# Kernel optimization log

Hardware: AMD Instinct MI355X
Metric: run time of the kernel (lower is better)

## Reference

```python
import jax, jax.numpy as jnp
import numpy as np

N = 100_000   # nodes
E = 1_600_000 # edges per graph
D = 64        # feature width
HA = 32       # attention hidden


def setup_inputs() -> dict:
    key = jax.random.key(0)
    ks = jax.random.split(key, 20)
    inp = {}
    inp["h"] = jax.random.normal(ks[0], (N, D), jnp.float32)
    inp["e_od"] = jax.random.normal(ks[1], (E, D), jnp.float32)
    inp["e_ad"] = jax.random.normal(ks[2], (E, D), jnp.float32)
    inp["src_od"] = jax.random.randint(ks[3], (E,), 0, N)
    inp["dst_od"] = jax.random.randint(ks[4], (E,), 0, N)
    inp["src_ad"] = jax.random.randint(ks[5], (E,), 0, N)
    inp["dst_ad"] = jax.random.randint(ks[6], (E,), 0, N)
    s = 1.0 / np.sqrt(D).astype(np.float32)
    # stacked params: index 0 = OD graph, index 1 = AD graph
    inp["W_src"]  = jax.random.normal(ks[7],  (2, D, D), jnp.float32) * s
    inp["W_dst"]  = jax.random.normal(ks[8],  (2, D, D), jnp.float32) * s
    inp["W_edge"] = jax.random.normal(ks[9],  (2, D, D), jnp.float32) * s
    inp["b_msg"]  = jnp.zeros((2, D), jnp.float32)
    inp["W_self"] = jax.random.normal(ks[10], (2, D, D), jnp.float32) * s
    inp["W_agg"]  = jax.random.normal(ks[11], (2, D, D), jnp.float32) * s
    inp["b_node"] = jnp.zeros((2, D), jnp.float32)
    # Attention (Aggregate_samedim): Linear(D->HA, bias) -> tanh -> Linear(HA->1, no bias)
    inp["attn_l1_w"] = jax.random.normal(ks[12], (D, HA), jnp.float32) * s
    inp["attn_l1_b"] = jnp.zeros((HA,), jnp.float32)
    inp["attn_l2_w"] = jax.random.normal(ks[13], (HA, 1), jnp.float32) * (1.0 / np.sqrt(HA).astype(np.float32))
    return inp


def reference(h, e_od, e_ad, src_od, dst_od, src_ad, dst_ad,
              W_src, W_dst, W_edge, b_msg, W_self, W_agg, b_node,
              attn_l1_w, attn_l1_b, attn_l2_w):
    def mpnn(i, e, src, dst):
        # edge message: gather src/dst node feats, small GEMMs, relu  [E, D]
        m = jax.nn.relu(h[src] @ W_src[i] + h[dst] @ W_dst[i] + e @ W_edge[i] + b_msg[i])
        # scatter-sum to destination nodes  [N, D]
        agg = jax.ops.segment_sum(m, dst, num_segments=N)
        # node update  [N, D]
        return jax.nn.relu(h @ W_self[i] + agg @ W_agg[i] + b_node[i])

    intra = mpnn(0, e_od, src_od, dst_od)  # OD graph node states
    inter = mpnn(1, e_ad, src_ad, dst_ad)  # AD graph node states
    # Aggregate_samedim: attention over the 2-way stack
    rep = jnp.stack([intra, inter], axis=1)               # [N, 2, D]
    w = jnp.tanh(rep @ attn_l1_w + attn_l1_b) @ attn_l2_w  # [N, 2, 1]
    beta = jax.nn.softmax(w, axis=1)
    return (beta * rep).sum(axis=1)                        # [N, D]
```

## Files before the change

kernel.cpp:

```cpp
#include <hip/hip_runtime.h>
#include <hip/hip_bf16.h>

using short8  = __attribute__((ext_vector_type(8))) short;
using ushort8 = __attribute__((ext_vector_type(8))) unsigned short;
using f32x4   = __attribute__((ext_vector_type(4))) float;
using fvec4   = __attribute__((ext_vector_type(4))) float;

#define CH 8192
#define XST 72

__device__ inline unsigned short f2bf(float x) {
  union { __hip_bfloat16 b; unsigned short u; } c;
  c.b = __float2bfloat16(x);
  return c.u;
}
__device__ inline float bf2f(unsigned short s) {
  return __uint_as_float(((unsigned int)s) << 16);
}
__device__ inline unsigned int pk2(float lo, float hi) {
  union { __hip_bfloat162 b; unsigned int u; } c;
  c.b = __float22bfloat162_rn(make_float2(lo, hi));
  return c.u;
}
__device__ inline short8 cvt8(fvec4 a, fvec4 b) {
  union { short8 s; unsigned int u[4]; } r;
  r.u[0] = pk2(a[0], a[1]);
  r.u[1] = pk2(a[2], a[3]);
  r.u[2] = pk2(b[0], b[1]);
  r.u[3] = pk2(b[2], b[3]);
  return r.s;
}

__device__ inline void load_bfrags_f32(const float* __restrict__ W, short8 bfr[2][4], int lane) {
  int l15 = lane & 15, lh = lane >> 4;
#pragma unroll
  for (int ks = 0; ks < 2; ++ks)
#pragma unroll
    for (int ct = 0; ct < 4; ++ct) {
      short8 v;
#pragma unroll
      for (int i = 0; i < 8; ++i)
        v[i] = (short)f2bf(W[(ks * 32 + lh * 8 + i) * 64 + ct * 16 + l15]);
      bfr[ks][ct] = v;
    }
}

__device__ inline void load_bfrags(const unsigned short* __restrict__ Wf, short8 bfr[2][4], int lane) {
#pragma unroll
  for (int ks = 0; ks < 2; ++ks)
#pragma unroll
    for (int ct = 0; ct < 4; ++ct) {
      union { ushort8 u; short8 s; } c;
      c.u = *reinterpret_cast<const ushort8*>(Wf + (((ks * 4 + ct) << 9) + (lane << 3)));
      bfr[ks][ct] = c.s;
    }
}

struct PrepArgs {
  const float* W[10];
};

__global__ __launch_bounds__(64) void prep_w_kernel(PrepArgs pw, unsigned short* __restrict__ Wf) {
  int z = blockIdx.x;
  int lane = threadIdx.x & 63;
  short8 bfr[2][4];
  load_bfrags_f32(pw.W[z], bfr, lane);
  unsigned short* dst = Wf + (size_t)z * 4096;
#pragma unroll
  for (int ks = 0; ks < 2; ++ks)
#pragma unroll
    for (int ct = 0; ct < 4; ++ct) {
      union { short8 s; ushort8 u; } c;
      c.s = bfr[ks][ct];
      *reinterpret_cast<ushort8*>(dst + (((ks * 4 + ct) << 9) + (lane << 3))) = c.u;
    }
}

struct ProjArgs {
  unsigned short* out[6];
};

__global__ __launch_bounds__(256) void proj_all_kernel(const float* __restrict__ h,
                                                       const unsigned short* __restrict__ Wf,
                                                       ProjArgs pa, int N) {
  int lane = threadIdx.x & 63;
  int wv = threadIdx.x >> 6;
  int rowbase = blockIdx.x * 256 + wv * 64;
  int l15 = lane & 15, lh = lane >> 4;

  short8 afr[4][2];
#pragma unroll
  for (int rt = 0; rt < 4; ++rt) {
    int row = rowbase + rt * 16 + l15;
    int rc = row < N ? row : 0;
    const fvec4* p = reinterpret_cast<const fvec4*>(h + (size_t)rc * 64);
#pragma unroll
    for (int ks = 0; ks < 2; ++ks)
      afr[rt][ks] = cvt8(p[ks * 8 + lh * 2], p[ks * 8 + lh * 2 + 1]);
  }

  for (int z = 0; z < 6; ++z) {
    short8 bfr[2][4];
    load_bfrags(Wf + (size_t)z * 4096, bfr, lane);
    unsigned short* __restrict__ out = pa.out[z];

    f32x4 acc[4][4];
#pragma unroll
    for (int rt = 0; rt < 4; ++rt)
#pragma unroll
      for (int ct = 0; ct < 4; ++ct) acc[rt][ct] = (f32x4){0.f, 0.f, 0.f, 0.f};

#pragma unroll
    for (int rt = 0; rt < 4; ++rt)
#pragma unroll
      for (int ks = 0; ks < 2; ++ks)
#pragma unroll
        for (int ct = 0; ct < 4; ++ct)
          acc[rt][ct] = __builtin_amdgcn_mfma_f32_16x16x32_bf16(afr[rt][ks], bfr[ks][ct], acc[rt][ct], 0, 0, 0);

#pragma unroll
    for (int rt = 0; rt < 4; ++rt)
#pragma unroll
      for (int rg = 0; rg < 4; ++rg) {
        int row = rowbase + rt * 16 + lh * 4 + rg;
        if (row < N) {
#pragma unroll
          for (int ct = 0; ct < 4; ++ct)
            out[(size_t)row * 64 + ct * 16 + l15] = f2bf(acc[rt][ct][rg]);
        }
      }
  }
}

__global__ __launch_bounds__(256) void hist_kernel(const int* __restrict__ dst0, const int* __restrict__ dst1,
                                                   int* __restrict__ counts, int E, int NBK) {
  __shared__ int hcnt[2048];
  int z = blockIdx.y;
  const int* __restrict__ dst = z ? dst1 : dst0;
  int t = threadIdx.x;
  for (int i = t; i < NBK; i += 256) hcnt[i] = 0;
  __syncthreads();
  int base = blockIdx.x * CH;
#pragma unroll 4
  for (int k = 0; k < CH / 256; ++k) {
    int i = base + k * 256 + t;
    if (i < E) atomicAdd(&hcnt[dst[i] >> 6], 1);
  }
  __syncthreads();
  for (int i = t; i < NBK; i += 256) {
    int c = hcnt[i];
    if (c) atomicAdd(&counts[(size_t)z * NBK + i], c);
  }
}

__global__ __launch_bounds__(1024) void scan_kernel(const int* __restrict__ counts, int* __restrict__ cursor,
                                                    int* __restrict__ gcur, int NBK) {
  int z = blockIdx.x;
  const int* c = counts + (size_t)z * NBK;
  __shared__ int lds[1024];
  int t = threadIdx.x;
  int carry = 0;
  for (int base = 0; base < NBK; base += 1024) {
    int i = base + t;
    int v = (i < NBK) ? c[i] : 0;
    lds[t] = v;
    __syncthreads();
    for (int off = 1; off < 1024; off <<= 1) {
      int x = (t >= off) ? lds[t - off] : 0;
      __syncthreads();
      lds[t] += x;
      __syncthreads();
    }
    if (i < NBK) {
      int excl = carry + lds[t] - v;
      cursor[(size_t)z * NBK + i] = excl;
      gcur[(size_t)z * NBK + i] = excl;
    }
    carry += lds[1023];
    __syncthreads();
  }
}

__global__ __launch_bounds__(256) void scatterA_kernel(
    const int* __restrict__ src0, const int* __restrict__ dst0,
    const int* __restrict__ src1, const int* __restrict__ dst1,
    int* __restrict__ gcur, int2* __restrict__ recs0, int2* __restrict__ recs1,
    int E, int NBK) {
  __shared__ int lcnt[2048];
  int z = blockIdx.y;
  const int* __restrict__ src = z ? src1 : src0;
  const int* __restrict__ dst = z ? dst1 : dst0;
  int2* __restrict__ recs = z ? recs1 : recs0;
  int t = threadIdx.x;
  for (int i = t; i < NBK; i += 256) lcnt[i] = 0;
  __syncthreads();
  int base = blockIdx.x * CH;
#pragma unroll 4
  for (int k = 0; k < CH / 256; ++k) {
    int i = base + k * 256 + t;
    if (i < E) atomicAdd(&lcnt[dst[i] >> 6], 1);
  }
  __syncthreads();
  for (int i = t; i < NBK; i += 256) {
    int c = lcnt[i];
    lcnt[i] = c ? atomicAdd(&gcur[(size_t)z * NBK + i], c) : 0;
  }
  __syncthreads();
#pragma unroll 4
  for (int k = 0; k < CH / 256; ++k) {
    int i = base + k * 256 + t;
    if (i < E) {
      int d = dst[i], s = src[i];
      int bin = d >> 6, dl = d & 63;
      int pos = atomicAdd(&lcnt[bin], 1);
      recs[pos] = make_int2(i | (bin << 21), s | (dl << 26));
    }
  }
}

__global__ __launch_bounds__(256) void sortB_kernel(int2* __restrict__ recs0, int2* __restrict__ recs1,
                                                    const int* __restrict__ cursor,
                                                    const int* __restrict__ counts, int NBK) {
  __shared__ int cnt_lds[64];
  __shared__ int cur_lds[64];
  int z = blockIdx.y;
  int b = blockIdx.x;
  int2* __restrict__ recs = z ? recs1 : recs0;
  int start = cursor[(size_t)z * NBK + b];
  int cnt = counts[(size_t)z * NBK + b];
  int t = threadIdx.x;

  for (int cbase = 0; cbase < cnt; cbase += 2048) {
    int ccnt = min(2048, cnt - cbase);
    int2 r[8];
    int dl[8];
    if (t < 64) cnt_lds[t] = 0;
    __syncthreads();
#pragma unroll
    for (int k = 0; k < 8; ++k) {
      int idx = k * 256 + t;
      if (idx < ccnt) {
        r[k] = recs[start + cbase + idx];
        dl[k] = ((unsigned)r[k].y) >> 26;
        atomicAdd(&cnt_lds[dl[k]], 1);
      }
    }
    __syncthreads();
    if (t < 64) {
      int c = cnt_lds[t];
      int x = c;
#pragma unroll
      for (int off = 1; off < 64; off <<= 1) {
        int y = __shfl_up(x, off);
        if (t >= off) x += y;
      }
      cur_lds[t] = x - c;
    }
    __syncthreads();
#pragma unroll
    for (int k = 0; k < 8; ++k) {
      int idx = k * 256 + t;
      if (idx < ccnt) {
        int pos = atomicAdd(&cur_lds[dl[k]], 1);
        recs[start + cbase + pos] = r[k];
      }
    }
    __syncthreads();
  }
}

__global__ __launch_bounds__(256) void edge_sorted_kernel(
    const float* __restrict__ e, const int2* __restrict__ recs,
    const unsigned short* __restrict__ Wf, const float* __restrict__ bmsg,
    const unsigned short* __restrict__ Psrc, const unsigned short* __restrict__ Pdst,
    float* __restrict__ agg, int E) {
  __shared__ unsigned short x_lds[4][64 * XST];

  int lane = threadIdx.x & 63;
  int wv = threadIdx.x >> 6;
  int base = (blockIdx.x * 4 + wv) * 64;
  if (base >= E) return;
  int l15 = lane & 15, lh = lane >> 4;
  unsigned short* xw = &x_lds[wv][0];

  int slot = base + lane;
  int el = 0, sl = 0, dl = 0;
  if (slot < E) {
    int2 rc = recs[slot];
    el = rc.x & 0x1FFFFF;
    sl = rc.y & 0x3FFFFFF;
    dl = (((rc.x >> 21) & 0x7FF) << 6) | (int)(((unsigned)rc.y) >> 26);
  }

  int myrow8 = lane >> 3, mychunk = lane & 7;
  ushort8 psv[8];
#pragma unroll
  for (int i = 0; i < 8; ++i) {
    int srow = __shfl(sl, i * 8 + myrow8);
    psv[i] = *reinterpret_cast<const ushort8*>(Psrc + ((size_t)srow << 6) + mychunk * 8);
  }
#pragma unroll
  for (int i = 0; i < 8; ++i)
    *reinterpret_cast<ushort8*>(xw + (i * 8 + myrow8) * XST + mychunk * 8) = psv[i];

  short8 bfr[2][4];
  load_bfrags(Wf, bfr, lane);

  f32x4 acc[4][4];
#pragma unroll
  for (int rt = 0; rt < 4; ++rt)
#pragma unroll
    for (int ct = 0; ct < 4; ++ct) acc[rt][ct] = (f32x4){0.f, 0.f, 0.f, 0.f};

#pragma unroll
  for (int rt = 0; rt < 4; ++rt) {
    int er = __shfl(el, rt * 16 + l15);
    const fvec4* pr = reinterpret_cast<const fvec4*>(e + ((size_t)er << 6));
#pragma unroll
    for (int ks = 0; ks < 2; ++ks) {
      short8 a = cvt8(pr[ks * 8 + lh * 2], pr[ks * 8 + lh * 2 + 1]);
#pragma unroll
      for (int ct = 0; ct < 4; ++ct)
        acc[rt][ct] = __builtin_amdgcn_mfma_f32_16x16x32_bf16(a, bfr[ks][ct], acc[rt][ct], 0, 0, 0);
    }
  }

  float bv[4];
#pragma unroll
  for (int ct = 0; ct < 4; ++ct) bv[ct] = bmsg[ct * 16 + l15];

  asm volatile("s_waitcnt lgkmcnt(0)" ::: "memory");
  __builtin_amdgcn_sched_barrier(0);

#pragma unroll
  for (int rt = 0; rt < 4; ++rt)
#pragma unroll
    for (int rg = 0; rg < 4; ++rg) {
      int row = rt * 16 + lh * 4 + rg;
#pragma unroll
      for (int ct = 0; ct < 4; ++ct) {
        int c = ct * 16 + l15;
        float v = acc[rt][ct][rg] + bf2f(xw[row * XST + c]) + bv[ct];
        xw[row * XST + c] = f2bf(v);
      }
    }

  asm volatile("s_waitcnt lgkmcnt(0)" ::: "memory");
  __builtin_amdgcn_sched_barrier(0);

  int dprev = __shfl_up(dl, 1);
  unsigned long long bnd = __ballot(lane > 0 && dl != dprev);
  int vrows = min(64, E - base);

  float racc = 0.f, pdv = 0.f;
  int dcur = -1;
#pragma unroll 4
  for (int r = 0; r < vrows; ++r) {
    bool newseg = (r == 0) || ((bnd >> r) & 1ull);
    if (newseg) {
      if (dcur >= 0) atomicAdd(&agg[(size_t)dcur * 64 + lane], racc);
      dcur = __shfl(dl, r);
      racc = 0.f;
      pdv = bf2f(Pdst[(size_t)dcur * 64 + lane]);
    }
    racc += fmaxf(bf2f(xw[r * XST + lane]) + pdv, 0.f);
  }
  if (dcur >= 0) atomicAdd(&agg[(size_t)dcur * 64 + lane], racc);
}

struct NodeArgs {
  const float* agg[2];
  const unsigned short* T[2];
  const float* bn[2];
  unsigned short* U[2];
};

__global__ __launch_bounds__(256) void node_kernel(const unsigned short* __restrict__ Wf,
                                                   NodeArgs na, int N) {
  int z = blockIdx.y;
  const float* __restrict__ agg = na.agg[z];
  const unsigned short* __restrict__ T = na.T[z];
  const float* __restrict__ bn = na.bn[z];
  unsigned short* __restrict__ U = na.U[z];
  int lane = threadIdx.x & 63;
  int wv = threadIdx.x >> 6;
  int rowbase = blockIdx.x * 256 + wv * 64;
  int l15 = lane & 15, lh = lane >> 4;

  short8 bfr[2][4];
  load_bfrags(Wf + (size_t)(8 + z) * 4096, bfr, lane);

  f32x4 acc[4][4];
#pragma unroll
  for (int rt = 0; rt < 4; ++rt)
#pragma unroll
    for (int ct = 0; ct < 4; ++ct) acc[rt][ct] = (f32x4){0.f, 0.f, 0.f, 0.f};

#pragma unroll
  for (int rt = 0; rt < 4; ++rt) {
    int row = rowbase + rt * 16 + l15;
    int rc = row < N ? row : 0;
    const fvec4* p = reinterpret_cast<const fvec4*>(agg + (size_t)rc * 64);
#pragma unroll
    for (int ks = 0; ks < 2; ++ks) {
      fvec4 p0 = p[ks * 8 + lh * 2], p1 = p[ks * 8 + lh * 2 + 1];
      short8 ahi = cvt8(p0, p1);
      fvec4 q0, q1;
#pragma unroll
      for (int i = 0; i < 4; ++i) {
        q0[i] = p0[i] - bf2f((unsigned short)ahi[i]);
        q1[i] = p1[i] - bf2f((unsigned short)ahi[i + 4]);
      }
      short8 alo = cvt8(q0, q1);
#pragma unroll
      for (int ct = 0; ct < 4; ++ct) {
        acc[rt][ct] = __builtin_amdgcn_mfma_f32_16x16x32_bf16(ahi, bfr[ks][ct], acc[rt][ct], 0, 0, 0);
        acc[rt][ct] = __builtin_amdgcn_mfma_f32_16x16x32_bf16(alo, bfr[ks][ct], acc[rt][ct], 0, 0, 0);
      }
    }
  }

  float bv[4];
#pragma unroll
  for (int ct = 0; ct < 4; ++ct) bv[ct] = bn[ct * 16 + l15];

#pragma unroll
  for (int rt = 0; rt < 4; ++rt)
#pragma unroll
    for (int rg = 0; rg < 4; ++rg) {
      int row = rowbase + rt * 16 + lh * 4 + rg;
      if (row < N) {
#pragma unroll
        for (int ct = 0; ct < 4; ++ct) {
          int c = ct * 16 + l15;
          float v = acc[rt][ct][rg] + bf2f(T[(size_t)row * 64 + c]) + bv[ct];
          U[(size_t)row * 64 + c] = f2bf(fmaxf(v, 0.0f));
        }
      }
    }
}

__global__ __launch_bounds__(256) void attn_kernel(
    const unsigned short* __restrict__ U0, const unsigned short* __restrict__ U1,
    const float* __restrict__ l1w, const float* __restrict__ l1b, const float* __restrict__ l2w,
    float* __restrict__ out, int N) {
  int t = threadIdx.x;
  int node = blockIdx.x * 64 + (t >> 2);
  int q = t & 3;
  if (node >= N) return;
  size_t b0 = (size_t)node * 64;

  float a0[8], a1[8];
#pragma unroll
  for (int i = 0; i < 8; ++i) { a0[i] = l1b[q * 8 + i]; a1[i] = a0[i]; }

  for (int k = 0; k < 64; ++k) {
    float u0 = bf2f(U0[b0 + k]);
    float u1 = bf2f(U1[b0 + k]);
#pragma unroll
    for (int i = 0; i < 8; ++i) {
      float w = l1w[k * 32 + q * 8 + i];
      a0[i] += u0 * w;
      a1[i] += u1 * w;
    }
  }
  float w0 = 0.f, w1 = 0.f;
#pragma unroll
  for (int i = 0; i < 8; ++i) {
    float l2 = l2w[q * 8 + i];
    w0 += tanhf(a0[i]) * l2;
    w1 += tanhf(a1[i]) * l2;
  }
  w0 += __shfl_xor(w0, 1, 4); w0 += __shfl_xor(w0, 2, 4);
  w1 += __shfl_xor(w1, 1, 4); w1 += __shfl_xor(w1, 2, 4);

  float m = fmaxf(w0, w1);
  float e0 = expf(w0 - m), e1 = expf(w1 - m);
  float inv = 1.0f / (e0 + e1);
  float be0 = e0 * inv, be1 = e1 * inv;

#pragma unroll
  for (int j = 0; j < 16; ++j) {
    int c = q * 16 + j;
    out[b0 + c] = be0 * bf2f(U0[b0 + c]) + be1 * bf2f(U1[b0 + c]);
  }
}

static inline size_t au(size_t x) { return (x + 255) & ~(size_t)255; }

extern "C" void kernel_launch(void* const* d_in, const int* in_sizes, int n_in,
                              void* d_out, int out_size, void* d_ws, size_t ws_size,
                              hipStream_t stream) {
  const float* h      = (const float*)d_in[0];
  const float* e_od   = (const float*)d_in[1];
  const float* e_ad   = (const float*)d_in[2];
  const int* src_od   = (const int*)d_in[3];
  const int* dst_od   = (const int*)d_in[4];
  const int* src_ad   = (const int*)d_in[5];
  const int* dst_ad   = (const int*)d_in[6];
  const float* W_src  = (const float*)d_in[7];
  const float* W_dst  = (const float*)d_in[8];
  const float* W_edge = (const float*)d_in[9];
  const float* b_msg  = (const float*)d_in[10];
  const float* W_self = (const float*)d_in[11];
  const float* W_agg  = (const float*)d_in[12];
  const float* b_node = (const float*)d_in[13];
  const float* l1w    = (const float*)d_in[14];
  const float* l1b    = (const float*)d_in[15];
  const float* l2w    = (const float*)d_in[16];
  float* out = (float*)d_out;

  int N = in_sizes[0] / 64;
  int E = in_sizes[1] / 64;
  int NBK = (N + 63) >> 6;

  char* ws = (char*)d_ws;
  size_t off = 0;
  int* counts = (int*)(ws + off);   off += au((size_t)2 * NBK * sizeof(int));
  float* agg0 = (float*)(ws + off); off += (size_t)N * 64 * sizeof(float);
  float* agg1 = (float*)(ws + off); off += (size_t)N * 64 * sizeof(float);
  size_t zero_bytes = off;
  int* cursor = (int*)(ws + off);   off += au((size_t)2 * NBK * sizeof(int));
  int* gcur   = (int*)(ws + off);   off += au((size_t)2 * NBK * sizeof(int));
  int2* recs0 = (int2*)(ws + off);  off += au((size_t)E * sizeof(int2));
  int2* recs1 = (int2*)(ws + off);  off += au((size_t)E * sizeof(int2));
  unsigned short* Wf = (unsigned short*)(ws + off); off += au((size_t)10 * 4096 * sizeof(unsigned short));
  size_t NP = au((size_t)N * 64 * sizeof(unsigned short));
  unsigned short* Psrc0 = (unsigned short*)(ws + off); off += NP;
  unsigned short* Pdst0 = (unsigned short*)(ws + off); off += NP;
  unsigned short* Psrc1 = (unsigned short*)(ws + off); off += NP;
  unsigned short* Pdst1 = (unsigned short*)(ws + off); off += NP;
  unsigned short* T0    = (unsigned short*)(ws + off); off += NP;
  unsigned short* T1    = (unsigned short*)(ws + off); off += NP;
  unsigned short* U0 = Psrc0;
  unsigned short* U1 = Psrc1;

  hipMemsetAsync(ws, 0, zero_bytes, stream);

  PrepArgs pw;
  pw.W[0] = W_src;         pw.W[1] = W_dst;
  pw.W[2] = W_src + 4096;  pw.W[3] = W_dst + 4096;
  pw.W[4] = W_self;        pw.W[5] = W_self + 4096;
  pw.W[6] = W_edge;        pw.W[7] = W_edge + 4096;
  pw.W[8] = W_agg;         pw.W[9] = W_agg + 4096;
  prep_w_kernel<<<10, 64, 0, stream>>>(pw, Wf);

  int nb = (N + 255) / 256;
  ProjArgs pa;
  pa.out[0] = Psrc0;
  pa.out[1] = Pdst0;
  pa.out[2] = Psrc1;
  pa.out[3] = Pdst1;
  pa.out[4] = T0;
  pa.out[5] = T1;
  proj_all_kernel<<<nb, 256, 0, stream>>>(h, Wf, pa, N);

  int nch = (E + CH - 1) / CH;
  hist_kernel<<<dim3(nch, 2), 256, 0, stream>>>(dst_od, dst_ad, counts, E, NBK);
  scan_kernel<<<2, 1024, 0, stream>>>(counts, cursor, gcur, NBK);
  scatterA_kernel<<<dim3(nch, 2), 256, 0, stream>>>(src_od, dst_od, src_ad, dst_ad, gcur,
                                                    recs0, recs1, E, NBK);
  sortB_kernel<<<dim3(NBK, 2), 256, 0, stream>>>(recs0, recs1, cursor, counts, NBK);

  int tiles = (E + 63) / 64;
  int eb = (tiles + 3) / 4;
  edge_sorted_kernel<<<eb, 256, 0, stream>>>(e_od, recs0, Wf + 6 * 4096, b_msg,
                                             Psrc0, Pdst0, agg0, E);
  edge_sorted_kernel<<<eb, 256, 0, stream>>>(e_ad, recs1, Wf + 7 * 4096, b_msg + 64,
                                             Psrc1, Pdst1, agg1, E);

  NodeArgs na;
  na.agg[0] = agg0; na.T[0] = T0; na.bn[0] = b_node;      na.U[0] = U0;
  na.agg[1] = agg1; na.T[1] = T1; na.bn[1] = b_node + 64; na.U[1] = U1;
  node_kernel<<<dim3(nb, 2), 256, 0, stream>>>(Wf, na, N);

  attn_kernel<<<(N + 63) / 64, 256, 0, stream>>>(U0, U1, l1w, l1b, l2w, out, N);
}
```

Before: 530.2 us.

## Fold Psrc add into MFMA via identity, swizzle LDS, merge both edge graphs

The edge kernel no longer stages gathered Psrc rows through LDS and re-adds them in a scalar pass. Instead it feeds them as A operands to extra MFMAs against an identity B fragment, and it seeds the accumulators with the bias. The result goes to LDS once, packed as bf16 in a transposed XOR-swizzled layout, and each lane reads its column back as vectors before a fully unrolled segment reduction. Both graphs now run in one launch using blockIdx.y. This removes one LDS read-modify-write round, bank conflicts and a launch, at the cost of extra MFMA work and more registers.

```diff
diff --git a/kernel.cpp b/kernel.cpp
--- a/kernel.cpp
+++ b/kernel.cpp
@@ -7,7 +7,6 @@
 using fvec4   = __attribute__((ext_vector_type(4))) float;
 
 #define CH 8192
-#define XST 72
 
 __device__ inline unsigned short f2bf(float x) {
   union { __hip_bfloat16 b; unsigned short u; } c;
@@ -269,12 +268,25 @@
   }
 }
 
-__global__ __launch_bounds__(256) void edge_sorted_kernel(
-    const float* __restrict__ e, const int2* __restrict__ recs,
-    const unsigned short* __restrict__ Wf, const float* __restrict__ bmsg,
-    const unsigned short* __restrict__ Psrc, const unsigned short* __restrict__ Pdst,
-    float* __restrict__ agg, int E) {
-  __shared__ unsigned short x_lds[4][64 * XST];
+struct EdgeArgs {
+  const float* e[2];
+  const int2* recs[2];
+  const unsigned short* We[2];
+  const float* bmsg[2];
+  const unsigned short* Ps[2];
+  const unsigned short* Pd[2];
+  float* agg[2];
+};
+
+__global__ __launch_bounds__(256) void edge_sorted_kernel(EdgeArgs ea, int E) {
+  __shared__ unsigned short x_lds[4][64 * 64];
+
+  int z = blockIdx.y;
+  const float* __restrict__ e = ea.e[z];
+  const int2* __restrict__ recs = ea.recs[z];
+  const unsigned short* __restrict__ Psrc = ea.Ps[z];
+  const unsigned short* __restrict__ Pdst = ea.Pd[z];
+  float* __restrict__ agg = ea.agg[z];
 
   int lane = threadIdx.x & 63;
   int wv = threadIdx.x >> 6;
@@ -292,61 +304,73 @@
     dl = (((rc.x >> 21) & 0x7FF) << 6) | (int)(((unsigned)rc.y) >> 26);
   }
 
-  int myrow8 = lane >> 3, mychunk = lane & 7;
-  ushort8 psv[8];
-#pragma unroll
-  for (int i = 0; i < 8; ++i) {
-    int srow = __shfl(sl, i * 8 + myrow8);
-    psv[i] = *reinterpret_cast<const ushort8*>(Psrc + ((size_t)srow << 6) + mychunk * 8);
-  }
-#pragma unroll
-  for (int i = 0; i < 8; ++i)
-    *reinterpret_cast<ushort8*>(xw + (i * 8 + myrow8) * XST + mychunk * 8) = psv[i];
-
   short8 bfr[2][4];
-  load_bfrags(Wf, bfr, lane);
-
+  load_bfrags(ea.We[z], bfr, lane);
+
+  short8 idf[2];
+#pragma unroll
+  for (int half = 0; half < 2; ++half) {
+    short8 v;
+#pragma unroll
+    for (int i = 0; i < 8; ++i)
+      v[i] = (short)((lh * 8 + i == half * 16 + l15) ? 0x3F80 : 0);
+    idf[half] = v;
+  }
+
+  const float* bmsg = ea.bmsg[z];
   f32x4 acc[4][4];
 #pragma unroll
+  for (int ct = 0; ct < 4; ++ct) {
+    float b = bmsg[ct * 16 + l15];
+    f32x4 bb = (f32x4){b, b, b, b};
+#pragma unroll
+    for (int rt = 0; rt < 4; ++rt) acc[rt][ct] = bb;
+  }
+
+#pragma unroll
+  for (int rt = 0; rt < 4; ++rt) {
+    int sr = rt * 16 + l15;
+    int er = __shfl(el, sr);
+    int hr = __shfl(sl, sr);
+    const fvec4* pr = reinterpret_cast<const fvec4*>(e + ((size_t)er << 6));
+    const ushort8* ps = reinterpret_cast<const ushort8*>(Psrc + ((size_t)hr << 6));
+    short8 aE0 = cvt8(pr[lh * 2], pr[lh * 2 + 1]);
+    short8 aE1 = cvt8(pr[8 + lh * 2], pr[8 + lh * 2 + 1]);
+    union { ushort8 u; short8 s; } aP0, aP1;
+    aP0.u = ps[lh];
+    aP1.u = ps[4 + lh];
+#pragma unroll
+    for (int ct = 0; ct < 4; ++ct) {
+      acc[rt][ct] = __builtin_amdgcn_mfma_f32_16x16x32_bf16(aE0, bfr[0][ct], acc[rt][ct], 0, 0, 0);
+      acc[rt][ct] = __builtin_amdgcn_mfma_f32_16x16x32_bf16(aE1, bfr[1][ct], acc[rt][ct], 0, 0, 0);
+    }
+    acc[rt][0] = __builtin_amdgcn_mfma_f32_16x16x32_bf16(aP0.s, idf[0], acc[rt][0], 0, 0, 0);
+    acc[rt][1] = __builtin_amdgcn_mfma_f32_16x16x32_bf16(aP0.s, idf[1], acc[rt][1], 0, 0, 0);
+    acc[rt][2] = __builtin_amdgcn_mfma_f32_16x16x32_bf16(aP1.s, idf[0], acc[rt][2], 0, 0, 0);
+    acc[rt][3] = __builtin_amdgcn_mfma_f32_16x16x32_bf16(aP1.s, idf[1], acc[rt][3], 0, 0, 0);
+  }
+
+#pragma unroll
   for (int rt = 0; rt < 4; ++rt)
 #pragma unroll
-    for (int ct = 0; ct < 4; ++ct) acc[rt][ct] = (f32x4){0.f, 0.f, 0.f, 0.f};
-
-#pragma unroll
-  for (int rt = 0; rt < 4; ++rt) {
-    int er = __shfl(el, rt * 16 + l15);
-    const fvec4* pr = reinterpret_cast<const fvec4*>(e + ((size_t)er << 6));
-#pragma unroll
-    for (int ks = 0; ks < 2; ++ks) {
-      short8 a = cvt8(pr[ks * 8 + lh * 2], pr[ks * 8 + lh * 2 + 1]);
-#pragma unroll
-      for (int ct = 0; ct < 4; ++ct)
-        acc[rt][ct] = __builtin_amdgcn_mfma_f32_16x16x32_bf16(a, bfr[ks][ct], acc[rt][ct], 0, 0, 0);
-    }
-  }
-
-  float bv[4];
-#pragma unroll
-  for (int ct = 0; ct < 4; ++ct) bv[ct] = bmsg[ct * 16 + l15];
+    for (int ct = 0; ct < 4; ++ct) {
+      int col = ct * 16 + l15;
+      int byte = (col << 7) + ((rt * 32 + lh * 8) ^ ((col & 7) << 4));
+      uint2 d;
+      d.x = pk2(acc[rt][ct][0], acc[rt][ct][1]);
+      d.y = pk2(acc[rt][ct][2], acc[rt][ct][3]);
+      *reinterpret_cast<uint2*>(reinterpret_cast<char*>(xw) + byte) = d;
+    }
 
   asm volatile("s_waitcnt lgkmcnt(0)" ::: "memory");
   __builtin_amdgcn_sched_barrier(0);
 
-#pragma unroll
-  for (int rt = 0; rt < 4; ++rt)
-#pragma unroll
-    for (int rg = 0; rg < 4; ++rg) {
-      int row = rt * 16 + lh * 4 + rg;
-#pragma unroll
-      for (int ct = 0; ct < 4; ++ct) {
-        int c = ct * 16 + l15;
-        float v = acc[rt][ct][rg] + bf2f(xw[row * XST + c]) + bv[ct];
-        xw[row * XST + c] = f2bf(v);
-      }
-    }
-
-  asm volatile("s_waitcnt lgkmcnt(0)" ::: "memory");
-  __builtin_amdgcn_sched_barrier(0);
+  ushort8 xv[8];
+#pragma unroll
+  for (int i = 0; i < 8; ++i) {
+    int byte = (lane << 7) + ((i * 16) ^ ((lane & 7) << 4));
+    xv[i] = *reinterpret_cast<ushort8*>(reinterpret_cast<char*>(xw) + byte);
+  }
 
   int dprev = __shfl_up(dl, 1);
   unsigned long long bnd = __ballot(lane > 0 && dl != dprev);
@@ -354,8 +378,8 @@
 
   float racc = 0.f, pdv = 0.f;
   int dcur = -1;
-#pragma unroll 4
-  for (int r = 0; r < vrows; ++r) {
+#pragma unroll
+  for (int r = 0; r < 64; ++r) {
     bool newseg = (r == 0) || ((bnd >> r) & 1ull);
     if (newseg) {
       if (dcur >= 0) atomicAdd(&agg[(size_t)dcur * 64 + lane], racc);
@@ -363,7 +387,8 @@
       racc = 0.f;
       pdv = bf2f(Pdst[(size_t)dcur * 64 + lane]);
     }
-    racc += fmaxf(bf2f(xw[r * XST + lane]) + pdv, 0.f);
+    float v = fmaxf(bf2f(xv[r >> 3][r & 7]) + pdv, 0.f);
+    racc += (r < vrows) ? v : 0.f;
   }
   if (dcur >= 0) atomicAdd(&agg[(size_t)dcur * 64 + lane], racc);
 }
@@ -564,10 +589,12 @@
 
   int tiles = (E + 63) / 64;
   int eb = (tiles + 3) / 4;
-  edge_sorted_kernel<<<eb, 256, 0, stream>>>(e_od, recs0, Wf + 6 * 4096, b_msg,
-                                             Psrc0, Pdst0, agg0, E);
-  edge_sorted_kernel<<<eb, 256, 0, stream>>>(e_ad, recs1, Wf + 7 * 4096, b_msg + 64,
-                                             Psrc1, Pdst1, agg1, E);
+  EdgeArgs ea;
+  ea.e[0] = e_od;  ea.recs[0] = recs0; ea.We[0] = Wf + 6 * 4096; ea.bmsg[0] = b_msg;
+  ea.Ps[0] = Psrc0; ea.Pd[0] = Pdst0; ea.agg[0] = agg0;
+  ea.e[1] = e_ad;  ea.recs[1] = recs1; ea.We[1] = Wf + 7 * 4096; ea.bmsg[1] = b_msg + 64;
+  ea.Ps[1] = Psrc1; ea.Pd[1] = Pdst1; ea.agg[1] = agg1;
+  edge_sorted_kernel<<<dim3(eb, 2), 256, 0, stream>>>(ea, E);
 
   NodeArgs na;
   na.agg[0] = agg0; na.T[0] = T0; na.bn[0] = b_node;      na.U[0] = U0;
```

Result: no change. 529.5 us (-0.1%).
